# Kernel optimization log

Hardware: AMD Instinct MI355X
Metric: run time of the kernel (lower is better)

The kernel has to match this reference:

```python
import jax, jax.numpy as jnp
import numpy as np

LOG_DUR_SCALE = 2.3  # durations ~ exp(U(0,2.3)) - 1, avg ~3 frames/phoneme


def setup_inputs() -> dict:
    key = jax.random.key(0)
    k1, k2 = jax.random.split(key)
    B, S, D = 32, 512, 384
    x = jax.random.normal(k1, (B, S, D), dtype=jnp.float32)
    log_duration_prediction = jax.random.uniform(k2, (B, S), dtype=jnp.float32) * LOG_DUR_SCALE
    return {"x": x, "log_duration_prediction": log_duration_prediction, "max_len": 3072}


def reference(x, log_duration_prediction, max_len):
    # duration_rounded = clamp(round(exp(logd) - 1), min=0)
    duration_rounded = jnp.clip(jnp.round(jnp.exp(log_duration_prediction) - 1.0), 0.0)
    dur = duration_rounded.astype(jnp.int32)                      # [B, S]
    cum = jnp.cumsum(dur, axis=1)                                 # [B, S] end offsets
    mel_len = jnp.minimum(cum[:, -1], max_len)                    # [B]
    t = jnp.arange(max_len, dtype=jnp.int32)                      # [T]
    # source index for output frame t: first phoneme whose cumulative end > t
    idx = jax.vmap(lambda c: jnp.searchsorted(c, t, side="right"))(cum)  # [B, T]
    idx = jnp.clip(idx, 0, x.shape[1] - 1)
    out = jnp.take_along_axis(x, idx[..., None], axis=1)          # [B, T, D]
    valid = t[None, :] < mel_len[:, None]                         # [B, T]
    out = jnp.where(valid[..., None], out, jnp.zeros((), out.dtype))
    mel_mask = ~valid  # get_mask_from_lengths: True at padding positions
    return out, duration_rounded, mel_len.astype(jnp.int32), mel_mask
```

## Files before the change

kernel.cpp:

```cpp
#include <hip/hip_runtime.h>

#define B 32
#define S 512
#define D 384
#define T 3072
#define FPB 32
#define D4 (D/4)
#define NTHREADS 256

typedef float f32x4 __attribute__((ext_vector_type(4)));

#define OFF_OUT  0
#define OFF_DUR  (B*T*D)
#define OFF_MLEN (OFF_DUR + B*S)
#define OFF_MASK (OFF_MLEN + B)

__global__ __launch_bounds__(NTHREADS) void upsample_kernel(
    const float* __restrict__ x, const float* __restrict__ logd,
    const int* __restrict__ max_len_p, float* __restrict__ outp)
{
    __shared__ int cum_s[S];
    __shared__ int wsum[NTHREADS / 64];
    __shared__ int sidx[FPB];
    __shared__ int mlen_sh;

    const int b   = blockIdx.y;
    const int t0  = blockIdx.x * FPB;
    const int tid = threadIdx.x;
    const int lane = tid & 63;
    const int wave = tid >> 6;

    const int s0 = tid * 2;
    const float* ldrow = logd + b * S;
    float ld0 = ldrow[s0], ld1 = ldrow[s0 + 1];
    float dr0 = fmaxf(rintf(expf(ld0) - 1.0f), 0.0f);
    float dr1 = fmaxf(rintf(expf(ld1) - 1.0f), 0.0f);
    int d1 = (int)dr1;
    int pairsum = (int)dr0 + d1;

    int v = pairsum;
    #pragma unroll
    for (int off = 1; off < 64; off <<= 1) {
        int u = __shfl_up(v, off, 64);
        if (lane >= off) v += u;
    }
    if (lane == 63) wsum[wave] = v;
    __syncthreads();
    if (tid == 0) {
        int acc = 0;
        #pragma unroll
        for (int w = 0; w < NTHREADS / 64; ++w) { int t = wsum[w]; wsum[w] = acc; acc += t; }
    }
    __syncthreads();
    const int inc  = v + wsum[wave];
    cum_s[s0]     = inc - d1;
    cum_s[s0 + 1] = inc;

    if (blockIdx.x == 0) {
        outp[OFF_DUR + b * S + s0]     = dr0;
        outp[OFF_DUR + b * S + s0 + 1] = dr1;
    }
    if (tid == NTHREADS - 1) mlen_sh = min(inc, max_len_p[0]);
    __syncthreads();
    const int mlen = mlen_sh;
    if (blockIdx.x == 0 && tid == 0) outp[OFF_MLEN + b] = (float)mlen;

    if (tid < FPB) {
        const int t = t0 + tid;
        int lo = 0;
        if (t < mlen) {
            int hi = S;
            while (lo < hi) {
                int mid = (lo + hi) >> 1;
                if (cum_s[mid] <= t) lo = mid + 1; else hi = mid;
            }
            if (lo > S - 1) lo = S - 1;
        }
        sidx[tid] = lo;
        __builtin_nontemporal_store((t < mlen) ? 0.0f : 1.0f,
                                    &outp[OFF_MASK + (size_t)b * T + t]);
    }
    __syncthreads();

    const f32x4* x4 = (const f32x4*)(x + (size_t)b * S * D);
    f32x4* o4 = (f32x4*)(outp + OFF_OUT + (size_t)b * T * D + (size_t)t0 * D);

    #pragma unroll
    for (int i = 0; i < (FPB * D4) / NTHREADS; ++i) {
        int w = tid + i * NTHREADS;
        int f = w / D4;
        int e = w - f * D4;
        int t = t0 + f;
        f32x4 val = (f32x4)(0.f);
        if (t < mlen) val = x4[(size_t)sidx[f] * D4 + e];
        __builtin_nontemporal_store(val, &o4[(size_t)f * D4 + e]);
    }
}

extern "C" void kernel_launch(void* const* d_in, const int* in_sizes, int n_in,
                              void* d_out, int out_size, void* d_ws, size_t ws_size,
                              hipStream_t stream) {
    const float* x      = (const float*)d_in[0];
    const float* logd   = (const float*)d_in[1];
    const int*   maxlen = (const int*)d_in[2];
    float* out = (float*)d_out;

    upsample_kernel<<<dim3(T / FPB, B), NTHREADS, 0, stream>>>(x, logd, maxlen, out);
}
```

Before: 36.41 us.

## Double frames per block, flatten grid, add fast paths for padded and full tiles

Each block now handles 64 frames instead of 32 and uses a 1D grid, which halves the number of blocks that each redo the per-row duration scan. Blocks whose whole tile lies past mel_len write zeros and exit without running the binary search or reading x. Fully valid tiles skip the per-element bounds check. Nontemporal stores are replaced by ordinary stores, which changes how the large output write interacts with the cache.

```diff
diff --git a/kernel.cpp b/kernel.cpp
--- a/kernel.cpp
+++ b/kernel.cpp
@@ -4,9 +4,10 @@
 #define S 512
 #define D 384
 #define T 3072
-#define FPB 32
+#define FPB 64
 #define D4 (D/4)
-#define NTHREADS 256
+#define NT 256
+#define BPR (T/FPB)
 
 typedef float f32x4 __attribute__((ext_vector_type(4)));
 
@@ -15,30 +16,28 @@
 #define OFF_MLEN (OFF_DUR + B*S)
 #define OFF_MASK (OFF_MLEN + B)
 
-__global__ __launch_bounds__(NTHREADS) void upsample_kernel(
+__global__ __launch_bounds__(NT) void upsample_kernel(
     const float* __restrict__ x, const float* __restrict__ logd,
     const int* __restrict__ max_len_p, float* __restrict__ outp)
 {
     __shared__ int cum_s[S];
-    __shared__ int wsum[NTHREADS / 64];
+    __shared__ int wsum[NT / 64];
     __shared__ int sidx[FPB];
     __shared__ int mlen_sh;
 
-    const int b   = blockIdx.y;
-    const int t0  = blockIdx.x * FPB;
+    const int bid = blockIdx.x;
+    const int b   = bid / BPR;
+    const int t0  = (bid % BPR) * FPB;
     const int tid = threadIdx.x;
     const int lane = tid & 63;
     const int wave = tid >> 6;
 
     const int s0 = tid * 2;
     const float* ldrow = logd + b * S;
-    float ld0 = ldrow[s0], ld1 = ldrow[s0 + 1];
-    float dr0 = fmaxf(rintf(expf(ld0) - 1.0f), 0.0f);
-    float dr1 = fmaxf(rintf(expf(ld1) - 1.0f), 0.0f);
+    float dr0 = fmaxf(rintf(expf(ldrow[s0])     - 1.0f), 0.0f);
+    float dr1 = fmaxf(rintf(expf(ldrow[s0 + 1]) - 1.0f), 0.0f);
     int d1 = (int)dr1;
-    int pairsum = (int)dr0 + d1;
-
-    int v = pairsum;
+    int v = (int)dr0 + d1;
     #pragma unroll
     for (int off = 1; off < 64; off <<= 1) {
         int u = __shfl_up(v, off, 64);
@@ -49,21 +48,37 @@
     if (tid == 0) {
         int acc = 0;
         #pragma unroll
-        for (int w = 0; w < NTHREADS / 64; ++w) { int t = wsum[w]; wsum[w] = acc; acc += t; }
+        for (int w = 0; w < NT / 64; ++w) { int t = wsum[w]; wsum[w] = acc; acc += t; }
     }
     __syncthreads();
-    const int inc  = v + wsum[wave];
+    const int inc = v + wsum[wave];
     cum_s[s0]     = inc - d1;
     cum_s[s0 + 1] = inc;
+    if (tid == NT - 1) mlen_sh = min(inc, max_len_p[0]);
 
-    if (blockIdx.x == 0) {
+    if (bid % BPR == 0) {
         outp[OFF_DUR + b * S + s0]     = dr0;
         outp[OFF_DUR + b * S + s0 + 1] = dr1;
     }
-    if (tid == NTHREADS - 1) mlen_sh = min(inc, max_len_p[0]);
     __syncthreads();
     const int mlen = mlen_sh;
-    if (blockIdx.x == 0 && tid == 0) outp[OFF_MLEN + b] = (float)mlen;
+    if (bid % BPR == 0 && tid == 0) outp[OFF_MLEN + b] = (float)mlen;
+
+    if (tid < FPB) {
+        const int t = t0 + tid;
+        outp[OFF_MASK + (size_t)b * T + t] = (t < mlen) ? 0.0f : 1.0f;
+    }
+
+    f32x4* o4 = (f32x4*)(outp + OFF_OUT + (size_t)b * T * D + (size_t)t0 * D);
+
+    if (t0 >= mlen) {
+        #pragma unroll
+        for (int i = 0; i < (FPB * D4) / NT; ++i) {
+            int w = tid + i * NT;
+            o4[w] = (f32x4)(0.f);
+        }
+        return;
+    }
 
     if (tid < FPB) {
         const int t = t0 + tid;
@@ -77,23 +92,31 @@
             if (lo > S - 1) lo = S - 1;
         }
         sidx[tid] = lo;
-        __builtin_nontemporal_store((t < mlen) ? 0.0f : 1.0f,
-                                    &outp[OFF_MASK + (size_t)b * T + t]);
     }
     __syncthreads();
 
     const f32x4* x4 = (const f32x4*)(x + (size_t)b * S * D);
-    f32x4* o4 = (f32x4*)(outp + OFF_OUT + (size_t)b * T * D + (size_t)t0 * D);
+
+    if (t0 + FPB <= mlen) {
+        #pragma unroll
+        for (int i = 0; i < (FPB * D4) / NT; ++i) {
+            int w = tid + i * NT;
+            int f = w / D4;
+            int e = w - f * D4;
+            o4[w] = x4[(size_t)sidx[f] * D4 + e];
+        }
+        return;
+    }
 
     #pragma unroll
-    for (int i = 0; i < (FPB * D4) / NTHREADS; ++i) {
-        int w = tid + i * NTHREADS;
+    for (int i = 0; i < (FPB * D4) / NT; ++i) {
+        int w = tid + i * NT;
         int f = w / D4;
         int e = w - f * D4;
         int t = t0 + f;
         f32x4 val = (f32x4)(0.f);
         if (t < mlen) val = x4[(size_t)sidx[f] * D4 + e];
-        __builtin_nontemporal_store(val, &o4[(size_t)f * D4 + e]);
+        o4[w] = val;
     }
 }
 
@@ -105,5 +128,5 @@
     const int*   maxlen = (const int*)d_in[2];
     float* out = (float*)d_out;
 
-    upsample_kernel<<<dim3(T / FPB, B), NTHREADS, 0, stream>>>(x, logd, maxlen, out);
+    upsample_kernel<<<BPR * B, NT, 0, stream>>>(x, logd, maxlen, out);
 }
```

Result: faster. 30.06 us (-17.4%).
